# Kernel tuning notes

Measured on AMD Instinct MI355X. Metric: run time of the kernel, lower is better.

Reference implementation:

```python
import jax, jax.numpy as jnp
import numpy as np

N = 50000      # nodes
E = 800000     # edges (before self loops)
DIN = 128      # input feature dim
H = 2          # attention heads
C = 64         # per-head hidden channels (hidden_dim)
HC = H * C     # 128, concat output width of each GATv2 layer
DOUT = 4       # NUM_LANES
NEG = 0.2      # GATv2 default negative_slope


def _w(key, fan_in, shape):
    return jax.random.normal(key, shape, dtype=jnp.float32) * (1.0 / np.sqrt(fan_in))


def setup_inputs() -> dict:
    key = jax.random.key(0)
    ks = jax.random.split(key, 32)
    inp = {
        "x": jax.random.normal(ks[0], (N, DIN), dtype=jnp.float32),
        "edge_index": jax.random.randint(ks[1], (2, E), 0, N, dtype=jnp.int64),
    }
    # layer 1: DIN -> H*C
    inp["W1l"] = _w(ks[2], DIN, (DIN, HC)); inp["b1l"] = jnp.zeros((HC,), jnp.float32)
    inp["W1r"] = _w(ks[3], DIN, (DIN, HC)); inp["b1r"] = jnp.zeros((HC,), jnp.float32)
    inp["att1"] = _w(ks[4], C, (H, C));     inp["bias1"] = jnp.zeros((HC,), jnp.float32)
    # layer 2: H*C -> H*C
    inp["W2l"] = _w(ks[5], HC, (HC, HC));   inp["b2l"] = jnp.zeros((HC,), jnp.float32)
    inp["W2r"] = _w(ks[6], HC, (HC, HC));   inp["b2r"] = jnp.zeros((HC,), jnp.float32)
    inp["att2"] = _w(ks[7], C, (H, C));     inp["bias2"] = jnp.zeros((HC,), jnp.float32)
    # layer 3: H*C -> H*C
    inp["W3l"] = _w(ks[8], HC, (HC, HC));   inp["b3l"] = jnp.zeros((HC,), jnp.float32)
    inp["W3r"] = _w(ks[9], HC, (HC, HC));   inp["b3r"] = jnp.zeros((HC,), jnp.float32)
    inp["att3"] = _w(ks[10], C, (H, C));    inp["bias3"] = jnp.zeros((HC,), jnp.float32)
    # output linear
    inp["Wout"] = _w(ks[11], HC, (HC, DOUT)); inp["bout"] = jnp.zeros((DOUT,), jnp.float32)
    return inp


def gat_layer(x, src, dst, Wl, bl, Wr, br, att, bias):
    # GATv2Conv, concat=True, add_self_loops already in src/dst.
    n = x.shape[0]
    h, c = att.shape
    xl = (x @ Wl + bl).reshape(n, h, c)   # source transform
    xr = (x @ Wr + br).reshape(n, h, c)   # target transform
    m = xl[src] + xr[dst]                               # [Etot, H, C]
    e = jnp.sum(jax.nn.leaky_relu(m, NEG) * att, -1)    # [Etot, H]
    emax = jax.ops.segment_max(e, dst, num_segments=n)  # segment softmax over in-edges
    p = jnp.exp(e - emax[dst])
    denom = jax.ops.segment_sum(p, dst, num_segments=n)
    alpha = p / denom[dst]                              # [Etot, H]
    out = jax.ops.segment_sum(alpha[:, :, None] * xl[src], dst, num_segments=n)
    return out.reshape(n, h * c) + bias


def reference(x, edge_index, W1l, b1l, W1r, b1r, att1, bias1,
              W2l, b2l, W2r, b2r, att2, bias2,
              W3l, b3l, W3r, b3r, att3, bias3, Wout, bout):
    n = x.shape[0]
    loop = jnp.arange(n, dtype=edge_index.dtype)
    src = jnp.concatenate([edge_index[0], loop])  # add self loops (PyG default)
    dst = jnp.concatenate([edge_index[1], loop])
    h = jax.nn.relu(gat_layer(x, src, dst, W1l, b1l, W1r, b1r, att1, bias1))
    h = jax.nn.relu(gat_layer(h, src, dst, W2l, b2l, W2r, b2r, att2, bias2))
    h = jax.nn.relu(gat_layer(h, src, dst, W3l, b3l, W3r, b3r, att3, bias3))
    return h @ Wout + bout
```

## Files before the change

kernel.cpp:

```cpp
#include <hip/hip_runtime.h>
#include <math.h>

#define DIN  128
#define HC   128
#define NEG  0.2f

typedef __attribute__((ext_vector_type(4))) float f32x4;
typedef __attribute__((ext_vector_type(8))) _Float16 half8;
typedef __attribute__((ext_vector_type(2))) _Float16 half2v;

__device__ __forceinline__ int colOf(int p) {
    return ((p >> 5) * 2 + (p & 1)) * 16 + ((p & 31) >> 1);
}

template <int CTRL>
__device__ __forceinline__ float dpp_xadd(float x) {
    int r = __builtin_amdgcn_update_dpp(0, __float_as_int(x), CTRL, 0xF, 0xF, true);
    return x + __int_as_float(r);
}
__device__ __forceinline__ float rowsum8(float x) {
    x = dpp_xadd<0xB1>(x);
    x = dpp_xadd<0x4E>(x);
    x = dpp_xadd<0x141>(x);
    return x;
}
__device__ __forceinline__ float rowsum16(float x) {
    x = dpp_xadd<0xB1>(x);
    x = dpp_xadd<0x4E>(x);
    x = dpp_xadd<0x141>(x);
    x = dpp_xadd<0x140>(x);
    return x;
}

__global__ void hist_kernel(const int* __restrict__ ei, int E, int N,
                            int* __restrict__ counts) {
    int i = blockIdx.x * blockDim.x + threadIdx.x;
    int Etot = E + N;
    if (i >= Etot) return;
    int dst = (i < E) ? ei[E + i] : (i - E);
    if (dst < 0 || dst >= N) return;
    atomicAdd(&counts[dst], 1);
}

__global__ void scan_kernel(const int* __restrict__ counts,
                            int* __restrict__ rowptr,
                            int* __restrict__ cursor, int n) {
    __shared__ int wsum[16];
    const int PER = 52;
    int tid  = threadIdx.x;
    int lane = tid & 63, wid = tid >> 6;
    int base = tid * PER;

    int4 vals[13];
    if (base + PER <= n) {
        #pragma unroll
        for (int j = 0; j < 13; ++j)
            vals[j] = *(const int4*)&counts[base + j * 4];
    } else {
        #pragma unroll
        for (int j = 0; j < 13; ++j) {
            int b = base + j * 4;
            vals[j].x = (b + 0 < n) ? counts[b + 0] : 0;
            vals[j].y = (b + 1 < n) ? counts[b + 1] : 0;
            vals[j].z = (b + 2 < n) ? counts[b + 2] : 0;
            vals[j].w = (b + 3 < n) ? counts[b + 3] : 0;
        }
    }
    int tsum = 0;
    #pragma unroll
    for (int j = 0; j < 13; ++j)
        tsum += vals[j].x + vals[j].y + vals[j].z + vals[j].w;

    int x = tsum;
    #pragma unroll
    for (int off = 1; off < 64; off <<= 1) {
        int y = __shfl_up(x, off, 64);
        if (lane >= off) x += y;
    }
    if (lane == 63) wsum[wid] = x;
    __syncthreads();
    if (tid < 16) {
        int w = wsum[tid];
        #pragma unroll
        for (int off = 1; off < 16; off <<= 1) {
            int y = __shfl_up(w, off, 64);
            if (tid >= off) w += y;
        }
        wsum[tid] = w;
    }
    __syncthreads();

    int run = (wid ? wsum[wid - 1] : 0) + (x - tsum);
    if (base + PER <= n) {
        #pragma unroll
        for (int j = 0; j < 13; ++j) {
            int4 r;
            r.x = run; run += vals[j].x;
            r.y = run; run += vals[j].y;
            r.z = run; run += vals[j].z;
            r.w = run; run += vals[j].w;
            *(int4*)&rowptr[base + j * 4] = r;
            *(int4*)&cursor[base + j * 4] = r;
        }
    } else {
        #pragma unroll
        for (int j = 0; j < 13; ++j) {
            int b = base + j * 4;
            if (b + 0 < n) { rowptr[b + 0] = run; cursor[b + 0] = run; } run += vals[j].x;
            if (b + 1 < n) { rowptr[b + 1] = run; cursor[b + 1] = run; } run += vals[j].y;
            if (b + 2 < n) { rowptr[b + 2] = run; cursor[b + 2] = run; } run += vals[j].z;
            if (b + 3 < n) { rowptr[b + 3] = run; cursor[b + 3] = run; } run += vals[j].w;
        }
    }
    if (tid == 1023) rowptr[n] = run;
}

__global__ void scatter_kernel(const int* __restrict__ ei, int E, int N,
                               int* __restrict__ cursor,
                               int* __restrict__ esrc) {
    int i = blockIdx.x * blockDim.x + threadIdx.x;
    int Etot = E + N;
    if (i >= Etot) return;
    int src = (i < E) ? ei[i]     : (i - E);
    int dst = (i < E) ? ei[E + i] : (i - E);
    if (dst < 0 || dst >= N || src < 0 || src >= N) return;
    int pos = atomicAdd(&cursor[dst], 1);
    esrc[pos] = src;
}

__global__ __launch_bounds__(256) void prep_w16(
        const float* __restrict__ W1l, const float* __restrict__ W1r,
        const float* __restrict__ W2l, const float* __restrict__ W2r,
        const float* __restrict__ W3l, const float* __restrict__ W3r,
        _Float16* __restrict__ w16) {
    int m = blockIdx.y;
    const float* W = (m == 0) ? W1l : (m == 1) ? W1r : (m == 2) ? W2l
                   : (m == 3) ? W2r : (m == 4) ? W3l : W3r;
    int t = blockIdx.x * 256 + threadIdx.x;
    int kb = t >> 9, nf = (t >> 6) & 7, l = t & 63;
    int col = nf * 16 + (l & 15);
    int k0  = kb * 32 + (l >> 4) * 8;
    size_t ob = ((size_t)m * 2048 + t) * 8;
    #pragma unroll
    for (int j = 0; j < 8; ++j) {
        int k = k0 + j;
        int krow = (m >= 2) ? colOf(k) : k;
        w16[ob + j] = (_Float16)W[(size_t)krow * 128 + col];
    }
}

#define GEMM_BODY(A_LOAD)                                                     \
    const _Float16* hpl = W16 + ((size_t)(matbase + 0) * 16384);              \
    const _Float16* hpr = W16 + ((size_t)(matbase + 1) * 16384);              \
    int tid = threadIdx.x;                                                    \
    int w   = tid >> 6;                                                       \
    int l   = tid & 63;                                                       \
    int m15 = l & 15, g = l >> 4;                                             \
    int rowbase = blockIdx.x * 32 + (w >> 1) * 16;                            \
    int nfb     = (w & 1) * 4;                                                \
    f32x4 accl[4], accr[4];                                                   \
    _Pragma("unroll")                                                         \
    for (int i = 0; i < 4; ++i) {                                             \
        accl[i] = (f32x4){0.f, 0.f, 0.f, 0.f};                                \
        accr[i] = (f32x4){0.f, 0.f, 0.f, 0.f};                                \
    }                                                                         \
    _Pragma("unroll")                                                         \
    for (int kb = 0; kb < 4; ++kb) {                                          \
        int arow = rowbase + m15;                                             \
        half8 a16 = (half8)(_Float16)0.f;                                     \
        A_LOAD                                                                \
        _Pragma("unroll")                                                     \
        for (int nfi = 0; nfi < 4; ++nfi) {                                   \
            int nf = nfb + nfi;                                               \
            size_t off = (((size_t)kb * 8 + nf) * 64 + l) * 8;                \
            half8 b_l = *(const half8*)&hpl[off];                             \
            half8 b_r = *(const half8*)&hpr[off];                             \
            accl[nfi] = __builtin_amdgcn_mfma_f32_16x16x32_f16(a16, b_l, accl[nfi], 0, 0, 0); \
            accr[nfi] = __builtin_amdgcn_mfma_f32_16x16x32_f16(a16, b_r, accr[nfi], 0, 0, 0); \
        }                                                                     \
    }                                                                         \
    float vbl[4], vbr[4];                                                     \
    _Pragma("unroll")                                                         \
    for (int nfi = 0; nfi < 4; ++nfi) {                                       \
        vbl[nfi] = bl[(nfb + nfi) * 16 + m15];                                \
        vbr[nfi] = br[(nfb + nfi) * 16 + m15];                                \
    }                                                                         \
    _Pragma("unroll")                                                         \
    for (int a2 = 0; a2 < 2; ++a2) {                                          \
        int a = (nfb >> 1) + a2;                                              \
        _Pragma("unroll")                                                     \
        for (int r = 0; r < 4; ++r) {                                         \
            int row = rowbase + g * 4 + r;                                    \
            if (row >= nrows) continue;                                       \
            size_t off = (size_t)row * 128 + a * 32 + m15 * 2;                \
            half2v pl, pr;                                                    \
            pl[0] = (_Float16)(accl[2 * a2][r]     + vbl[2 * a2]);            \
            pl[1] = (_Float16)(accl[2 * a2 + 1][r] + vbl[2 * a2 + 1]);        \
            pr[0] = (_Float16)(accr[2 * a2][r]     + vbr[2 * a2]);            \
            pr[1] = (_Float16)(accr[2 * a2 + 1][r] + vbr[2 * a2 + 1]);        \
            *(half2v*)&xlh[off] = pl;                                         \
            *(half2v*)&xrh[off] = pr;                                         \
        }                                                                     \
    }

__global__ __launch_bounds__(256) void gemm_f16_from_f32(
        const float* __restrict__ X, const _Float16* __restrict__ W16,
        int matbase, const float* __restrict__ bl, const float* __restrict__ br,
        _Float16* __restrict__ xlh, _Float16* __restrict__ xrh, int nrows) {
    GEMM_BODY(
        if (arow < nrows) {
            const float* xp = &X[(size_t)arow * 128 + kb * 32 + g * 8];
            float4 x0 = *(const float4*)xp;
            float4 x1 = *(const float4*)(xp + 4);
            a16[0] = (_Float16)x0.x; a16[1] = (_Float16)x0.y;
            a16[2] = (_Float16)x0.z; a16[3] = (_Float16)x0.w;
            a16[4] = (_Float16)x1.x; a16[5] = (_Float16)x1.y;
            a16[6] = (_Float16)x1.z; a16[7] = (_Float16)x1.w;
        }
    )
}

__global__ __launch_bounds__(256) void gemm_f16_from_f16(
        const _Float16* __restrict__ X, const _Float16* __restrict__ W16,
        int matbase, const float* __restrict__ bl, const float* __restrict__ br,
        _Float16* __restrict__ xlh, _Float16* __restrict__ xrh, int nrows) {
    GEMM_BODY(
        if (arow < nrows)
            a16 = *(const half8*)&X[(size_t)arow * 128 + kb * 32 + g * 8];
    )
}

__global__ __launch_bounds__(256) void gat_aggregate(
        const _Float16* __restrict__ xlh, const _Float16* __restrict__ xrh,
        const int* __restrict__ rowptr, const int* __restrict__ esrc,
        const float* __restrict__ att, const float* __restrict__ bias,
        _Float16* __restrict__ hout, int n, int do_relu,
        const float* __restrict__ Wout, const float* __restrict__ bout,
        float* __restrict__ out4) {
    int node = (int)((blockIdx.x * blockDim.x + threadIdx.x) >> 6);
    int lane = threadIdx.x & 63;
    if (node >= n) return;
    int g    = lane >> 4;
    int gl   = lane & 15;
    int pos0 = gl * 8;

    half8 xr8 = *(const half8*)&xrh[(size_t)node * 128 + pos0];
    float xrf[8], atp[8], atn[8];
    #pragma unroll
    for (int i = 0; i < 8; ++i) {
        float a = att[colOf(pos0 + i)];
        atp[i] = a;
        atn[i] = NEG * a;
        xrf[i] = (float)xr8[i];
    }

    float s = 0.f;
    float acc[8];
    #pragma unroll
    for (int i = 0; i < 8; ++i) acc[i] = 0.f;

    int pbeg = rowptr[node], pend = rowptr[node + 1];
    int p = pbeg + g;
    bool v0 = p < pend;
    bool v1 = p + 4 < pend;
    half8 r0 = (half8)(_Float16)0.f, r1 = r0;
    if (v0) r0 = *(const half8*)&xlh[(size_t)esrc[p] * 128 + pos0];
    if (v1) r1 = *(const half8*)&xlh[(size_t)esrc[p + 4] * 128 + pos0];

    while (v0) {
        bool v2 = p + 8 < pend;
        half8 r2 = (half8)(_Float16)0.f;
        if (v2) r2 = *(const half8*)&xlh[(size_t)esrc[p + 8] * 128 + pos0];

        float av[8], t = 0.f;
        #pragma unroll
        for (int i = 0; i < 8; ++i) {
            av[i] = (float)r0[i];
            float v = av[i] + xrf[i];
            t += v * (v > 0.f ? atp[i] : atn[i]);
        }
        t = rowsum8(t);
        float pp = __expf(fminf(t, 80.f));
        s += pp;
        #pragma unroll
        for (int i = 0; i < 8; ++i) acc[i] += pp * av[i];

        r0 = r1; r1 = r2; v0 = v1; v1 = v2; p += 4;
    }

    #pragma unroll
    for (int off = 16; off <= 32; off <<= 1) {
        s += __shfl_xor(s, off, 64);
        #pragma unroll
        for (int i = 0; i < 8; ++i) acc[i] += __shfl_xor(acc[i], off, 64);
    }

    float inv = 1.f / s;

    if (out4) {
        float o[8];
        #pragma unroll
        for (int i = 0; i < 8; ++i) {
            o[i] = acc[i] * inv + bias[colOf(pos0 + i)];
            if (do_relu) o[i] = fmaxf(o[i], 0.f);
        }
        float p0 = 0.f, p1 = 0.f, p2 = 0.f, p3 = 0.f;
        #pragma unroll
        for (int i = 0; i < 8; ++i) {
            float4 wv = *(const float4*)&Wout[colOf(pos0 + i) * 4];
            p0 += o[i] * wv.x; p1 += o[i] * wv.y;
            p2 += o[i] * wv.z; p3 += o[i] * wv.w;
        }
        p0 = rowsum16(p0); p1 = rowsum16(p1);
        p2 = rowsum16(p2); p3 = rowsum16(p3);
        if (lane == 0) {
            float4 ov = make_float4(p0 + bout[0], p1 + bout[1],
                                    p2 + bout[2], p3 + bout[3]);
            *(float4*)&out4[(size_t)node * 4] = ov;
        }
        return;
    }

    if (g == 0) {
        half8 oh;
        #pragma unroll
        for (int i = 0; i < 8; ++i) {
            float o = acc[i] * inv + bias[colOf(pos0 + i)];
            if (do_relu) o = fmaxf(o, 0.f);
            oh[i] = (_Float16)o;
        }
        *(half8*)&hout[(size_t)node * 128 + pos0] = oh;
    }
}

extern "C" void kernel_launch(void* const* d_in, const int* in_sizes, int n_in,
                              void* d_out, int out_size, void* d_ws,
                              size_t ws_size, hipStream_t stream) {
    const float* x    = (const float*)d_in[0];
    const int*   ei   = (const int*)  d_in[1];
    const float* W1l  = (const float*)d_in[2];
    const float* b1l  = (const float*)d_in[3];
    const float* W1r  = (const float*)d_in[4];
    const float* b1r  = (const float*)d_in[5];
    const float* att1 = (const float*)d_in[6];
    const float* bias1= (const float*)d_in[7];
    const float* W2l  = (const float*)d_in[8];
    const float* b2l  = (const float*)d_in[9];
    const float* W2r  = (const float*)d_in[10];
    const float* b2r  = (const float*)d_in[11];
    const float* att2 = (const float*)d_in[12];
    const float* bias2= (const float*)d_in[13];
    const float* W3l  = (const float*)d_in[14];
    const float* b3l  = (const float*)d_in[15];
    const float* W3r  = (const float*)d_in[16];
    const float* b3r  = (const float*)d_in[17];
    const float* att3 = (const float*)d_in[18];
    const float* bias3= (const float*)d_in[19];
    const float* Wout = (const float*)d_in[20];
    const float* bout = (const float*)d_in[21];

    int N    = in_sizes[0] / DIN;
    int E    = in_sizes[1] / 2;
    int Etot = E + N;

    char* base = (char*)d_ws;
    _Float16* h16 = (_Float16*)base;      base += (size_t)N * HC * 2;
    _Float16* xlh = (_Float16*)base;      base += (size_t)N * HC * 2;
    _Float16* xrh = (_Float16*)base;      base += (size_t)N * HC * 2;
    _Float16* w16 = (_Float16*)base;      base += 6 * 16384 * 2;
    int* esrc   = (int*)base;             base += (size_t)Etot * 4;
    int* rowptr = (int*)base;             base += (size_t)(((N + 1) + 3) & ~3) * 4;
    int* cursor = (int*)base;             base += (size_t)N * 4;
    int* counts = (int*)base;

    hipMemsetAsync(counts, 0, (size_t)N * sizeof(int), stream);
    hist_kernel<<<(Etot + 255) / 256, 256, 0, stream>>>(ei, E, N, counts);
    scan_kernel<<<1, 1024, 0, stream>>>(counts, rowptr, cursor, N);
    scatter_kernel<<<(Etot + 255) / 256, 256, 0, stream>>>(ei, E, N, cursor, esrc);
    prep_w16<<<dim3(8, 6), 256, 0, stream>>>(W1l, W1r, W2l, W2r, W3l, W3r, w16);

    int gemm_grid = (N + 31) / 32;
    int agg_grid  = (N + 3) / 4;

    gemm_f16_from_f32<<<gemm_grid, 256, 0, stream>>>(x, w16, 0, b1l, b1r, xlh, xrh, N);
    gat_aggregate<<<agg_grid, 256, 0, stream>>>(xlh, xrh, rowptr, esrc, att1, bias1,
                                                h16, N, 1, nullptr, nullptr, nullptr);
    gemm_f16_from_f16<<<gemm_grid, 256, 0, stream>>>(h16, w16, 2, b2l, b2r, xlh, xrh, N);
    gat_aggregate<<<agg_grid, 256, 0, stream>>>(xlh, xrh, rowptr, esrc, att2, bias2,
                                                h16, N, 1, nullptr, nullptr, nullptr);
    gemm_f16_from_f16<<<gemm_grid, 256, 0, stream>>>(h16, w16, 4, b3l, b3r, xlh, xrh, N);
    gat_aggregate<<<agg_grid, 256, 0, stream>>>(xlh, xrh, rowptr, esrc, att3, bias3,
                                                nullptr, N, 1, Wout, bout,
                                                (float*)d_out);
}
```

Measured before the change: 323.1 us.

## Sort nodes by in-degree so aggregate waves process similar-degree nodes

Adds a counting sort of nodes by in-degree (histogram, scan, scatter kernels) and makes each aggregation wave look up its node through the resulting permutation. Grouping nodes of similar degree in the same block is meant to reduce load imbalance and idle waves. In exchange it adds three small kernels with atomics, an extra indirection, and less locality in node-indexed reads and writes.

```diff
diff --git a/kernel.cpp b/kernel.cpp
--- a/kernel.cpp
+++ b/kernel.cpp
@@ -126,6 +126,44 @@
     if (dst < 0 || dst >= N || src < 0 || src >= N) return;
     int pos = atomicAdd(&cursor[dst], 1);
     esrc[pos] = src;
+}
+
+__global__ void deg_hist_kernel(const int* __restrict__ counts, int n,
+                                int* __restrict__ dbins) {
+    int i = blockIdx.x * blockDim.x + threadIdx.x;
+    if (i >= n) return;
+    int d = counts[i];
+    atomicAdd(&dbins[d > 255 ? 255 : d], 1);
+}
+
+__global__ void deg_scan_kernel(const int* __restrict__ dbins,
+                                int* __restrict__ dcur) {
+    int lane = threadIdx.x;
+    int4 v = *(const int4*)&dbins[lane * 4];
+    int ssum = v.x + v.y + v.z + v.w;
+    int x = ssum;
+    #pragma unroll
+    for (int off = 1; off < 64; off <<= 1) {
+        int y = __shfl_up(x, off, 64);
+        if (lane >= off) x += y;
+    }
+    int run = x - ssum;
+    int4 r;
+    r.x = run;
+    r.y = r.x + v.x;
+    r.z = r.y + v.y;
+    r.w = r.z + v.z;
+    *(int4*)&dcur[lane * 4] = r;
+}
+
+__global__ void deg_scatter_kernel(const int* __restrict__ counts, int n,
+                                   int* __restrict__ dcur,
+                                   int* __restrict__ norder) {
+    int i = blockIdx.x * blockDim.x + threadIdx.x;
+    if (i >= n) return;
+    int d = counts[i];
+    int pos = atomicAdd(&dcur[d > 255 ? 255 : d], 1);
+    norder[pos] = i;
 }
 
 __global__ __launch_bounds__(256) void prep_w16(
@@ -233,13 +271,15 @@
 __global__ __launch_bounds__(256) void gat_aggregate(
         const _Float16* __restrict__ xlh, const _Float16* __restrict__ xrh,
         const int* __restrict__ rowptr, const int* __restrict__ esrc,
+        const int* __restrict__ norder,
         const float* __restrict__ att, const float* __restrict__ bias,
         _Float16* __restrict__ hout, int n, int do_relu,
         const float* __restrict__ Wout, const float* __restrict__ bout,
         float* __restrict__ out4) {
-    int node = (int)((blockIdx.x * blockDim.x + threadIdx.x) >> 6);
+    int widx = (int)((blockIdx.x * blockDim.x + threadIdx.x) >> 6);
     int lane = threadIdx.x & 63;
-    if (node >= n) return;
+    if (widx >= n) return;
+    int node = norder[widx];
     int g    = lane >> 4;
     int gl   = lane & 15;
     int pos0 = gl * 8;
@@ -371,25 +411,34 @@
     int* esrc   = (int*)base;             base += (size_t)Etot * 4;
     int* rowptr = (int*)base;             base += (size_t)(((N + 1) + 3) & ~3) * 4;
     int* cursor = (int*)base;             base += (size_t)N * 4;
-    int* counts = (int*)base;
-
-    hipMemsetAsync(counts, 0, (size_t)N * sizeof(int), stream);
+    int* norder = (int*)base;             base += (size_t)N * 4;
+    int* dcur   = (int*)base;             base += 256 * 4;
+    int* counts = (int*)base;             base += (size_t)N * 4;
+    int* dbins  = (int*)base;             base += 256 * 4;
+
+    hipMemsetAsync(counts, 0, ((size_t)N + 256) * sizeof(int), stream);
     hist_kernel<<<(Etot + 255) / 256, 256, 0, stream>>>(ei, E, N, counts);
     scan_kernel<<<1, 1024, 0, stream>>>(counts, rowptr, cursor, N);
     scatter_kernel<<<(Etot + 255) / 256, 256, 0, stream>>>(ei, E, N, cursor, esrc);
+    deg_hist_kernel<<<(N + 255) / 256, 256, 0, stream>>>(counts, N, dbins);
+    deg_scan_kernel<<<1, 64, 0, stream>>>(dbins, dcur);
+    deg_scatter_kernel<<<(N + 255) / 256, 256, 0, stream>>>(counts, N, dcur, norder);
     prep_w16<<<dim3(8, 6), 256, 0, stream>>>(W1l, W1r, W2l, W2r, W3l, W3r, w16);
 
     int gemm_grid = (N + 31) / 32;
     int agg_grid  = (N + 3) / 4;
 
     gemm_f16_from_f32<<<gemm_grid, 256, 0, stream>>>(x, w16, 0, b1l, b1r, xlh, xrh, N);
-    gat_aggregate<<<agg_grid, 256, 0, stream>>>(xlh, xrh, rowptr, esrc, att1, bias1,
+    gat_aggregate<<<agg_grid, 256, 0, stream>>>(xlh, xrh, rowptr, esrc, norder,
+                                                att1, bias1,
                                                 h16, N, 1, nullptr, nullptr, nullptr);
     gemm_f16_from_f16<<<gemm_grid, 256, 0, stream>>>(h16, w16, 2, b2l, b2r, xlh, xrh, N);
-    gat_aggregate<<<agg_grid, 256, 0, stream>>>(xlh, xrh, rowptr, esrc, att2, bias2,
+    gat_aggregate<<<agg_grid, 256, 0, stream>>>(xlh, xrh, rowptr, esrc, norder,
+                                                att2, bias2,
                                                 h16, N, 1, nullptr, nullptr, nullptr);
     gemm_f16_from_f16<<<gemm_grid, 256, 0, stream>>>(h16, w16, 4, b3l, b3r, xlh, xrh, N);
-    gat_aggregate<<<agg_grid, 256, 0, stream>>>(xlh, xrh, rowptr, esrc, att3, bias3,
+    gat_aggregate<<<agg_grid, 256, 0, stream>>>(xlh, xrh, rowptr, esrc, norder,
+                                                att3, bias3,
                                                 nullptr, N, 1, Wout, bout,
                                                 (float*)d_out);
 }
```

Result: slower. 624.9 us (+93.4%).
